# Optimization experiments

Hardware: AMD Instinct MI355X
Metric: run time of the kernel (lower is better)

Reference implementation:

```python
import jax, jax.numpy as jnp
import numpy as np

WIN = 5          # ssim_window_size
SIGMA = 1.5      # Gaussian sigma used by the reference implementation
C1 = 0.01 ** 2
C2 = 0.03 ** 2
MS_WEIGHTS = jnp.array([0.0448, 0.2856, 0.3001, 0.2363, 0.1333], dtype=jnp.float32)


def make_window(num_channel, dtype):
    x = jnp.arange(WIN, dtype=jnp.float32) - (WIN // 2)
    g = jnp.exp(-(x ** 2) / (2.0 * SIGMA ** 2))
    g = g / g.sum()
    w2 = jnp.outer(g, g)
    return jnp.broadcast_to(w2, (num_channel, 1, WIN, WIN)).astype(dtype)


def dwconv(x, w):
    pad = WIN // 2
    return jax.lax.conv_general_dilated(
        x, w, window_strides=(1, 1), padding=[(pad, pad), (pad, pad)],
        dimension_numbers=('NCHW', 'OIHW', 'NCHW'),
        feature_group_count=x.shape[1])


def compute_ssim(img1, img2):
    w = make_window(img1.shape[1], img1.dtype)
    mu1 = dwconv(img1, w)
    mu2 = dwconv(img2, w)
    mu1_sq = mu1 * mu1
    mu2_sq = mu2 * mu2
    mu1_mu2 = mu1 * mu2
    sigma1_sq = dwconv(img1 * img1, w) - mu1_sq
    sigma2_sq = dwconv(img2 * img2, w) - mu2_sq
    sigma12 = dwconv(img1 * img2, w) - mu1_mu2
    ssim_map = ((2 * mu1_mu2 + C1) * (2 * sigma12 + C2)) / (
        (mu1_sq + mu2_sq + C1) * (sigma1_sq + sigma2_sq + C2))
    cs = jnp.mean((2.0 * sigma12 + C2) / (sigma1_sq + sigma2_sq + C2))
    return jnp.mean(ssim_map), cs


def avg_pool2(x):
    s = jax.lax.reduce_window(x, jnp.array(0, x.dtype), jax.lax.add,
                              (1, 1, 2, 2), (1, 1, 2, 2), 'VALID')
    return s / jnp.array(4, x.dtype)


def ms_ssim(img1, img2):
    levels = MS_WEIGHTS.shape[0]
    ssims, mcs = [], []
    for _ in range(levels):
        s, cs = compute_ssim(img1, img2)
        ssims.append(s)
        mcs.append(cs)
        img1 = avg_pool2(img1)
        img2 = avg_pool2(img2)
    ssims = (jnp.stack(ssims) + 1) / 2
    mcs = (jnp.stack(mcs) + 1) / 2
    pow1 = mcs ** MS_WEIGHTS
    pow2 = ssims ** MS_WEIGHTS
    return jnp.prod(pow1[:-1] * pow2[-1])


def setup_inputs() -> dict:
    key = jax.random.key(0)
    k1, k2 = jax.random.split(key)
    shape = (32, 3, 512, 512)
    img1 = jax.random.uniform(k1, shape, dtype=jnp.float32)
    img2 = jax.random.uniform(k2, shape, dtype=jnp.float32)
    return {"img1": img1, "img2": img2}


def reference(img1, img2):
    return ms_ssim(img1, img2)
```

## Files before the change

kernel.cpp:

```cpp
#include <hip/hip_runtime.h>
#include <math.h>


typedef float f2 __attribute__((ext_vector_type(2)));

#if __has_builtin(__builtin_elementwise_fma)
static __device__ __forceinline__ f2 vfma(f2 a, f2 b, f2 c) {
    return __builtin_elementwise_fma(a, b, c);
}
#else
static __device__ __forceinline__ f2 vfma(f2 a, f2 b, f2 c) {
    f2 d; d.x = __builtin_fmaf(a.x, b.x, c.x); d.y = __builtin_fmaf(a.y, b.y, c.y);
    return d;
}
#endif

#define C1F 0.0001f
#define C2F 0.0009f
#define GW0f 0.12007838f
#define GW1f 0.23388060f
#define GW2f 0.29208204f

#define HCONV(DST, VM, V01, V23) do { \
    const f2 t1_ = (VM) + (V23); \
    f2 mid_; mid_.x = (VM).y + (V01).y; mid_.y = (V01).x + (V23).x; \
    (DST) = vfma(G1v, mid_, vfma(G0v, t1_, G2v * (V01))); \
} while (0)

#define VCONV(OUT, WN, S0,S1,S2,S3,S4) do { \
    const f2 t_ = WN[S0] + WN[S4]; \
    const f2 u_ = WN[S1] + WN[S3]; \
    (OUT) = vfma(G1v, u_, vfma(G0v, t_, G2v * WN[S2])); \
} while (0)

#define ROW(J,S0,S1,S2,S3,S4) do { \
    const int i = i0 + (J); \
    if (i < iters) { \
        const int r = y0 + i - 2; \
        const bool rok = (unsigned)r < (unsigned)H; \
        f2 X01 = {0.f, 0.f}, X23 = {0.f, 0.f}; \
        f2 Z01 = {0.f, 0.f}, Z23 = {0.f, 0.f}; \
        if (rok && g01) { \
            const size_t ro_ = (size_t)r * W + c0; \
            X01 = *(const f2*)(p1 + ro_); \
            Z01 = *(const f2*)(p2 + ro_); \
        } \
        if (rok && g23) { \
            const size_t ro_ = (size_t)r * W + c0 + 2; \
            X23 = *(const f2*)(p1 + ro_); \
            Z23 = *(const f2*)(p2 + ro_); \
        } \
        f2 XM, ZM; \
        XM.x = __shfl_up(X01.x, 1); XM.y = __shfl_up(X01.y, 1); \
        ZM.x = __shfl_up(Z01.x, 1); ZM.y = __shfl_up(Z01.y, 1); \
        const f2 QM  = vfma(ZM,  ZM,  XM * XM); \
        const f2 Q01 = vfma(Z01, Z01, X01 * X01); \
        const f2 Q23 = vfma(Z23, Z23, X23 * X23); \
        const f2 PM  = XM * ZM; \
        const f2 P01 = X01 * Z01; \
        const f2 P23 = X23 * Z23; \
        HCONV(wa[(J)], XM, X01, X23); \
        HCONV(wb[(J)], ZM, Z01, Z23); \
        HCONV(wq[(J)], QM, Q01, Q23); \
        HCONV(wp[(J)], PM, P01, P23); \
        if (i >= 4) { \
            f2 Av, Bv, Qv, Pv; \
            VCONV(Av, wa, S0,S1,S2,S3,S4); \
            VCONV(Bv, wb, S0,S1,S2,S3,S4); \
            VCONV(Qv, wq, S0,S1,S2,S3,S4); \
            VCONV(Pv, wp, S0,S1,S2,S3,S4); \
            const f2 ABv   = Av * Bv; \
            const f2 A2B2v = vfma(Bv, Bv, Av * Av); \
            const f2 S12v  = vfma(TWOv, Pv - ABv, C2v); \
            const f2 SDENv = (Qv - A2B2v) + C2v; \
            const f2 D1v   = A2B2v + C1v; \
            const f2 N1v   = vfma(TWOv, ABv, C1v); \
            const f2 DENv  = D1v * SDENv; \
            f2 RDv; \
            RDv.x = __builtin_amdgcn_rcpf(DENv.x); \
            RDv.y = __builtin_amdgcn_rcpf(DENv.y); \
            const f2 SSv = N1v * S12v * RDv; \
            const f2 CCv = S12v * D1v * RDv; \
            if (vout) { ACCS += SSv; ACCC += CCv; } \
        } \
        if (q1 && (i & 1) && i >= 3 && i <= TROWS + 1 && vout) { \
            const f2 sx_ = X01 + PX; \
            const f2 sz_ = Z01 + PZ; \
            const size_t po_ = (size_t)(r >> 1) * WP + (c0 >> 1); \
            q1[po_] = (sx_.x + sx_.y) * 0.25f; \
            q2[po_] = (sz_.x + sz_.y) * 0.25f; \
        } \
        PX = X01; PZ = Z01; \
    } \
} while (0)

template<int TROWS, int WPB>
__global__ __launch_bounds__(WPB * 64)
void ssim_level_kernel(const float* __restrict__ img1,
                       const float* __restrict__ img2,
                       int H, int W, int SX, int SY,
                       float* __restrict__ pool1,
                       float* __restrict__ pool2,
                       double* __restrict__ block_out)
{
    const int lane = threadIdx.x & 63;
    const int wv   = threadIdx.x >> 6;
    const int w    = blockIdx.x * WPB + wv;

    const int spp   = SX * SY;
    const int plane = w / spp;
    const int rem   = w - plane * spp;
    const int sy    = rem / SX;
    const int sx    = rem - sy * SX;

    const int base = sx * 124;
    const int y0   = sy * TROWS;
    const int c0   = base - 2 + 2 * lane;
    const bool g01 = ((unsigned)c0 < (unsigned)W) && (lane < 63);
    const bool g23 = ((unsigned)(c0 + 2) < (unsigned)W) && (lane < 63);
    const bool vout = g01 && (lane >= 1);

    const float* p1 = img1 + (size_t)plane * H * W;
    const float* p2 = img2 + (size_t)plane * H * W;
    const int WP = W >> 1;
    float* q1 = pool1 ? pool1 + (size_t)plane * (H >> 1) * WP : nullptr;
    float* q2 = pool2 ? pool2 + (size_t)plane * (H >> 1) * WP : nullptr;

    const f2 G0v  = {GW0f, GW0f};
    const f2 G1v  = {GW1f, GW1f};
    const f2 G2v  = {GW2f, GW2f};
    const f2 C1v  = {C1F, C1F};
    const f2 C2v  = {C2F, C2F};
    const f2 TWOv = {2.f, 2.f};

    f2 wa[5], wb[5], wq[5], wp[5];
    f2 PX = {0.f, 0.f}, PZ = {0.f, 0.f};
    f2 ACCS = {0.f, 0.f}, ACCC = {0.f, 0.f};

    const int iters = TROWS + 4;
    for (int i0 = 0; i0 < iters; i0 += 5) {
        ROW(0, 1, 2, 3, 4, 0);
        ROW(1, 2, 3, 4, 0, 1);
        ROW(2, 3, 4, 0, 1, 2);
        ROW(3, 4, 0, 1, 2, 3);
        ROW(4, 0, 1, 2, 3, 4);
    }

    float accs = ACCS.x + ACCS.y;
    float accc = ACCC.x + ACCC.y;
    #pragma unroll
    for (int o = 32; o > 0; o >>= 1) {
        accs += __shfl_down(accs, o, 64);
        accc += __shfl_down(accc, o, 64);
    }

    __shared__ double sred[WPB][2];
    if (lane == 0) { sred[wv][0] = (double)accs; sred[wv][1] = (double)accc; }
    __syncthreads();
    if (threadIdx.x == 0) {
        double s = 0.0, c = 0.0;
        #pragma unroll
        for (int k = 0; k < WPB; ++k) { s += sred[k][0]; c += sred[k][1]; }
        block_out[2 * (size_t)blockIdx.x]     = s;
        block_out[2 * (size_t)blockIdx.x + 1] = c;
    }
}

static constexpr int NBLK[5] = {1920, 576, 384, 384, 384};
static constexpr int BOFF[5] = {0, 1920, 2496, 2880, 3264};

__global__ __launch_bounds__(1024)
void ssim_final_kernel(const double* __restrict__ bsum, float* __restrict__ out)
{
    __shared__ double partial[16][2];
    __shared__ double lvl[5][2];
    const double npx[5] = {96.0*512*512, 96.0*256*256, 96.0*128*128,
                           96.0*64*64,   96.0*32*32};
    const int tid = threadIdx.x, lane = tid & 63, wv = tid >> 6;

    for (int l = 0; l < 5; ++l) {
        double s = 0.0, c = 0.0;
        for (int k = tid; k < NBLK[l]; k += 1024) {
            s += bsum[2 * (size_t)(BOFF[l] + k)];
            c += bsum[2 * (size_t)(BOFF[l] + k) + 1];
        }
        #pragma unroll
        for (int o = 32; o > 0; o >>= 1) {
            s += __shfl_down(s, o, 64);
            c += __shfl_down(c, o, 64);
        }
        if (lane == 0) { partial[wv][0] = s; partial[wv][1] = c; }
        __syncthreads();
        if (tid == 0) {
            double ts = 0.0, tc = 0.0;
            for (int k = 0; k < 16; ++k) { ts += partial[k][0]; tc += partial[k][1]; }
            lvl[l][0] = ts / npx[l];
            lvl[l][1] = tc / npx[l];
        }
        __syncthreads();
    }
    if (tid == 0) {
        const double wgt[5] = {0.0448, 0.2856, 0.3001, 0.2363, 0.1333};
        double ssim4 = (lvl[4][0] + 1.0) * 0.5;
        double P = pow(ssim4, wgt[4]);
        double r = pow((lvl[0][1] + 1.0) * 0.5, wgt[0]) *
                   pow((lvl[1][1] + 1.0) * 0.5, wgt[1]) *
                   pow((lvl[2][1] + 1.0) * 0.5, wgt[2]) *
                   pow((lvl[3][1] + 1.0) * 0.5, wgt[3]);
        r *= P * P * P * P;
        out[0] = (float)r;
    }
}

extern "C" void kernel_launch(void* const* d_in, const int* in_sizes, int n_in,
                              void* d_out, int out_size, void* d_ws, size_t ws_size,
                              hipStream_t stream)
{
    const float* img1 = (const float*)d_in[0];
    const float* img2 = (const float*)d_in[1];
    float* out = (float*)d_out;

    char* ws = (char*)d_ws;
    double* wsum = (double*)ws;
    size_t off = 262144;
    const size_t P = 96;
    float* l1a = (float*)(ws + off); off += P * 256 * 256 * sizeof(float);
    float* l1b = (float*)(ws + off); off += P * 256 * 256 * sizeof(float);
    float* l2a = (float*)(ws + off); off += P * 128 * 128 * sizeof(float);
    float* l2b = (float*)(ws + off); off += P * 128 * 128 * sizeof(float);
    float* l3a = (float*)(ws + off); off += P * 64 * 64 * sizeof(float);
    float* l3b = (float*)(ws + off); off += P * 64 * 64 * sizeof(float);
    float* l4a = (float*)(ws + off); off += P * 32 * 32 * sizeof(float);
    float* l4b = (float*)(ws + off); off += P * 32 * 32 * sizeof(float);

    ssim_level_kernel<32, 4><<<1920, 256, 0, stream>>>(
        img1, img2, 512, 512, 5, 16, l1a, l1b, wsum + 2 * (size_t)BOFF[0]);
    ssim_level_kernel<32, 4><<<576, 256, 0, stream>>>(
        l1a, l1b, 256, 256, 3, 8, l2a, l2b, wsum + 2 * (size_t)BOFF[1]);
    ssim_level_kernel<16, 4><<<384, 256, 0, stream>>>(
        l2a, l2b, 128, 128, 2, 8, l3a, l3b, wsum + 2 * (size_t)BOFF[2]);
    ssim_level_kernel<16, 1><<<384, 64, 0, stream>>>(
        l3a, l3b, 64, 64, 1, 4, l4a, l4b, wsum + 2 * (size_t)BOFF[3]);
    ssim_level_kernel<8, 1><<<384, 64, 0, stream>>>(
        l4a, l4b, 32, 32, 1, 4, nullptr, nullptr, wsum + 2 * (size_t)BOFF[4]);

    ssim_final_kernel<<<1, 1024, 0, stream>>>(wsum, out);
}
```

Before: 322.7 us.

## Load column halos directly per lane instead of wave shuffles, retile all levels

Each lane now loads left, center and right float2 pairs itself, with masks at image edges, rather than taking the left neighbour through __shfl_up and spending two lanes on halo. Every lane of the wave then produces output, so a wave covers 128 columns instead of 124 and the strip grid becomes 4x16 on the top level. Tile heights, strips per level and block counts are changed for every level, and the small levels now use 4-wave blocks. The cost is redundant overlapping global loads, which should mostly hit cache, in exchange for dropping the shuffles, idle lanes and leftover tiles.

```diff
diff --git a/kernel.cpp b/kernel.cpp
--- a/kernel.cpp
+++ b/kernel.cpp
@@ -21,9 +21,9 @@
 #define GW1f 0.23388060f
 #define GW2f 0.29208204f
 
-#define HCONV(DST, VM, V01, V23) do { \
-    const f2 t1_ = (VM) + (V23); \
-    f2 mid_; mid_.x = (VM).y + (V01).y; mid_.y = (V01).x + (V23).x; \
+#define HCONV(DST, VL, V01, VR) do { \
+    const f2 t1_ = (VL) + (VR); \
+    f2 mid_; mid_.x = (VL).y + (V01).y; mid_.y = (V01).x + (VR).x; \
     (DST) = vfma(G1v, mid_, vfma(G0v, t1_, G2v * (V01))); \
 } while (0)
 
@@ -37,32 +37,28 @@
     const int i = i0 + (J); \
     if (i < iters) { \
         const int r = y0 + i - 2; \
-        const bool rok = (unsigned)r < (unsigned)H; \
-        f2 X01 = {0.f, 0.f}, X23 = {0.f, 0.f}; \
-        f2 Z01 = {0.f, 0.f}, Z23 = {0.f, 0.f}; \
-        if (rok && g01) { \
-            const size_t ro_ = (size_t)r * W + c0; \
-            X01 = *(const f2*)(p1 + ro_); \
-            Z01 = *(const f2*)(p2 + ro_); \
+        f2 XL = {0.f,0.f}, X01 = {0.f,0.f}, XR = {0.f,0.f}; \
+        f2 ZL = {0.f,0.f}, Z01 = {0.f,0.f}, ZR = {0.f,0.f}; \
+        if ((unsigned)r < (unsigned)H) { \
+            const float* r1_ = p1 + (size_t)r * (size_t)W; \
+            const float* r2_ = p2 + (size_t)r * (size_t)W; \
+            XL  = *(const f2*)(r1_ + offL) * mL; \
+            X01 = *(const f2*)(r1_ + offC); \
+            XR  = *(const f2*)(r1_ + offR) * mR; \
+            ZL  = *(const f2*)(r2_ + offL) * mL; \
+            Z01 = *(const f2*)(r2_ + offC); \
+            ZR  = *(const f2*)(r2_ + offR) * mR; \
         } \
-        if (rok && g23) { \
-            const size_t ro_ = (size_t)r * W + c0 + 2; \
-            X23 = *(const f2*)(p1 + ro_); \
-            Z23 = *(const f2*)(p2 + ro_); \
-        } \
-        f2 XM, ZM; \
-        XM.x = __shfl_up(X01.x, 1); XM.y = __shfl_up(X01.y, 1); \
-        ZM.x = __shfl_up(Z01.x, 1); ZM.y = __shfl_up(Z01.y, 1); \
-        const f2 QM  = vfma(ZM,  ZM,  XM * XM); \
-        const f2 Q01 = vfma(Z01, Z01, X01 * X01); \
-        const f2 Q23 = vfma(Z23, Z23, X23 * X23); \
-        const f2 PM  = XM * ZM; \
-        const f2 P01 = X01 * Z01; \
-        const f2 P23 = X23 * Z23; \
-        HCONV(wa[(J)], XM, X01, X23); \
-        HCONV(wb[(J)], ZM, Z01, Z23); \
-        HCONV(wq[(J)], QM, Q01, Q23); \
-        HCONV(wp[(J)], PM, P01, P23); \
+        const f2 QL = vfma(ZL,  ZL,  XL  * XL); \
+        const f2 QC = vfma(Z01, Z01, X01 * X01); \
+        const f2 QR = vfma(ZR,  ZR,  XR  * XR); \
+        const f2 PL = XL  * ZL; \
+        const f2 PC = X01 * Z01; \
+        const f2 PR = XR  * ZR; \
+        HCONV(wa[(J)], XL, X01, XR); \
+        HCONV(wb[(J)], ZL, Z01, ZR); \
+        HCONV(wq[(J)], QL, QC,  QR); \
+        HCONV(wp[(J)], PL, PC,  PR); \
         if (i >= 4) { \
             f2 Av, Bv, Qv, Pv; \
             VCONV(Av, wa, S0,S1,S2,S3,S4); \
@@ -81,9 +77,9 @@
             RDv.y = __builtin_amdgcn_rcpf(DENv.y); \
             const f2 SSv = N1v * S12v * RDv; \
             const f2 CCv = S12v * D1v * RDv; \
-            if (vout) { ACCS += SSv; ACCC += CCv; } \
+            if (gC) { ACCS += SSv; ACCC += CCv; } \
         } \
-        if (q1 && (i & 1) && i >= 3 && i <= TROWS + 1 && vout) { \
+        if (q1 && (i & 1) && i >= 3 && i <= TROWS + 1 && gC) { \
             const f2 sx_ = X01 + PX; \
             const f2 sz_ = Z01 + PZ; \
             const size_t po_ = (size_t)(r >> 1) * WP + (c0 >> 1); \
@@ -113,12 +109,17 @@
     const int sy    = rem / SX;
     const int sx    = rem - sy * SX;
 
-    const int base = sx * 124;
+    const int base = sx * 128;
     const int y0   = sy * TROWS;
-    const int c0   = base - 2 + 2 * lane;
-    const bool g01 = ((unsigned)c0 < (unsigned)W) && (lane < 63);
-    const bool g23 = ((unsigned)(c0 + 2) < (unsigned)W) && (lane < 63);
-    const bool vout = g01 && (lane >= 1);
+    const int c0   = base + 2 * lane;
+    const bool gC = (unsigned)c0 < (unsigned)W;
+    const bool gL = (c0 - 2) >= 0 && (c0 - 2) < W;
+    const bool gR = (c0 + 2) < W;
+    const int offL = gL ? (c0 - 2) : c0;
+    const int offC = gC ? c0 : 0;
+    const int offR = gR ? (c0 + 2) : 0;
+    const f2 mL = {gL ? 1.f : 0.f, gL ? 1.f : 0.f};
+    const f2 mR = {gR ? 1.f : 0.f, gR ? 1.f : 0.f};
 
     const float* p1 = img1 + (size_t)plane * H * W;
     const float* p2 = img2 + (size_t)plane * H * W;
@@ -166,8 +167,8 @@
     }
 }
 
-static constexpr int NBLK[5] = {1920, 576, 384, 384, 384};
-static constexpr int BOFF[5] = {0, 1920, 2496, 2880, 3264};
+static constexpr int NBLK[5] = {1536, 768, 384, 384, 192};
+static constexpr int BOFF[5] = {0, 1536, 2304, 2688, 3072};
 
 __global__ __launch_bounds__(1024)
 void ssim_final_kernel(const double* __restrict__ bsum, float* __restrict__ out)
@@ -233,16 +234,16 @@
     float* l4a = (float*)(ws + off); off += P * 32 * 32 * sizeof(float);
     float* l4b = (float*)(ws + off); off += P * 32 * 32 * sizeof(float);
 
-    ssim_level_kernel<32, 4><<<1920, 256, 0, stream>>>(
-        img1, img2, 512, 512, 5, 16, l1a, l1b, wsum + 2 * (size_t)BOFF[0]);
-    ssim_level_kernel<32, 4><<<576, 256, 0, stream>>>(
-        l1a, l1b, 256, 256, 3, 8, l2a, l2b, wsum + 2 * (size_t)BOFF[1]);
-    ssim_level_kernel<16, 4><<<384, 256, 0, stream>>>(
-        l2a, l2b, 128, 128, 2, 8, l3a, l3b, wsum + 2 * (size_t)BOFF[2]);
-    ssim_level_kernel<16, 1><<<384, 64, 0, stream>>>(
-        l3a, l3b, 64, 64, 1, 4, l4a, l4b, wsum + 2 * (size_t)BOFF[3]);
-    ssim_level_kernel<8, 1><<<384, 64, 0, stream>>>(
-        l4a, l4b, 32, 32, 1, 4, nullptr, nullptr, wsum + 2 * (size_t)BOFF[4]);
+    ssim_level_kernel<32, 4><<<1536, 256, 0, stream>>>(
+        img1, img2, 512, 512, 4, 16, l1a, l1b, wsum + 2 * (size_t)BOFF[0]);
+    ssim_level_kernel<16, 4><<<768, 256, 0, stream>>>(
+        l1a, l1b, 256, 256, 2, 16, l2a, l2b, wsum + 2 * (size_t)BOFF[1]);
+    ssim_level_kernel<8, 4><<<384, 256, 0, stream>>>(
+        l2a, l2b, 128, 128, 1, 16, l3a, l3b, wsum + 2 * (size_t)BOFF[2]);
+    ssim_level_kernel<4, 4><<<384, 256, 0, stream>>>(
+        l3a, l3b, 64, 64, 1, 16, l4a, l4b, wsum + 2 * (size_t)BOFF[3]);
+    ssim_level_kernel<4, 4><<<192, 256, 0, stream>>>(
+        l4a, l4b, 32, 32, 1, 8, nullptr, nullptr, wsum + 2 * (size_t)BOFF[4]);
 
     ssim_final_kernel<<<1, 1024, 0, stream>>>(wsum, out);
 }
```

After: 300.8 us. -6.8%, faster.
